# Kernel tuning notes

Measured on AMD Instinct MI355X. Metric: run time of the kernel, lower is better.

The kernel has to match this reference:

```python
import jax, jax.numpy as jnp
import numpy as np

TEMPERATURE = 8.0  # sqrt(head_dim=64)


def sparsemax(z):
    """Sparsemax along the last axis (Martins & Astudillo 2016)."""
    S = z.shape[-1]
    z_sorted = -jnp.sort(-z, axis=-1)            # descending sort
    cs = jnp.cumsum(z_sorted, axis=-1)
    ks = jnp.arange(1, S + 1, dtype=z.dtype)
    support = 1.0 + ks * z_sorted > cs           # entries in the support set
    k_sup = jnp.sum(support, axis=-1, keepdims=True)  # support size >= 1
    tau = (jnp.take_along_axis(cs, k_sup - 1, axis=-1) - 1.0) / k_sup.astype(z.dtype)
    return jnp.maximum(z - tau, 0.0)


def setup_inputs() -> dict:
    key = jax.random.key(0)
    kq, kk, kv, km = jax.random.split(key, 4)
    B, Lq, Lk, D = 64, 1024, 1024, 64
    q = jax.random.normal(kq, (B, Lq, D), dtype=jnp.float32)
    k = jax.random.normal(kk, (B, Lk, D), dtype=jnp.float32)
    v = jax.random.normal(kv, (B, Lk, D), dtype=jnp.float32)
    mask = jax.random.randint(km, (B, Lq, Lk), 0, 2).astype(bool)  # True = masked out
    return {"q": q, "k": k, "v": v, "mask": mask}


def reference(q, k, v, mask):
    # scores: [B, Lq, Lk]
    attn = jnp.einsum('bqd,bkd->bqk', q / TEMPERATURE, k)
    # mask out disallowed keys with -inf
    attn = jnp.where(mask, -jnp.inf, attn)
    # rows where ALL keys are masked: set scores to 0 (avoids NaN in sparsemax)
    inf_mask = jnp.all(mask, axis=2, keepdims=True)  # [B, Lq, 1]
    attn = jnp.where(inf_mask, 0.0, attn)
    attn = sparsemax(attn)
    # zero out fully-masked rows again (dropout has p=0.0 -> identity in eval)
    attn = jnp.where(inf_mask, 0.0, attn)
    out = jnp.einsum('bqk,bkd->bqd', attn, v)
    return (out, attn)
```

## Files before the change

kernel.cpp:

```cpp
#include <hip/hip_runtime.h>
#include <float.h>


#define BATCH    64
#define SEQQ     1024
#define SEQK     1024
#define DHEAD    64

typedef short short8 __attribute__((ext_vector_type(8)));
typedef float f32x4  __attribute__((ext_vector_type(4)));

__device__ __forceinline__ unsigned short bf16_rne(float f) {
    unsigned u = __float_as_uint(f);
    u += 0x7fffu + ((u >> 16) & 1u);
    return (unsigned short)(u >> 16);
}

__device__ __forceinline__ void cvt_hilo8(const float* fv, float scale,
                                          short8* hi, short8* lo) {
    #pragma unroll
    for (int j = 0; j < 8; ++j) {
        float f = fv[j] * scale;
        unsigned short hb = bf16_rne(f);
        float hf = __uint_as_float((unsigned)hb << 16);
        (*hi)[j] = (short)hb;
        (*lo)[j] = (short)bf16_rne(f - hf);
    }
}

__global__ void detect_mask_fmt(const unsigned char* __restrict__ m,
                                int* __restrict__ flag) {
    __shared__ int s_found;
    if (threadIdx.x == 0) s_found = 0;
    __syncthreads();
    int found = 0;
    for (int o = threadIdx.x; o < 65536; o += 256) {
        if ((o & 3) != 0 && m[o] != 0) found = 1;
    }
    if (found) atomicOr(&s_found, 1);
    __syncthreads();
    if (threadIdx.x == 0) *flag = s_found;
}

__global__ __launch_bounds__(256) void score_kernel(
        const float* __restrict__ q, const float* __restrict__ k,
        unsigned short* __restrict__ sbuf, int pitch) {
    const int lane = threadIdx.x & 63;
    const int wave = threadIdx.x >> 6;
    const int quad = lane >> 4;
    const int l15  = lane & 15;
    const int kt = blockIdx.x, qt = blockIdx.y, b = blockIdx.z;

    __shared__ unsigned short klds[2 * 128 * 64];

    const float* kbase = k + ((size_t)b * SEQK + kt * 128) * DHEAD;
    #pragma unroll
    for (int it = 0; it < 4; ++it) {
        int e   = threadIdx.x + 256 * it;
        int key = e >> 3, db = e & 7;
        const float4* src = (const float4*)(kbase + key * DHEAD + db * 8);
        float4 f0 = src[0], f1 = src[1];
        float fv[8] = {f0.x, f0.y, f0.z, f0.w, f1.x, f1.y, f1.z, f1.w};
        short8 hi, lo;
        cvt_hilo8(fv, 1.0f, &hi, &lo);
        int off = key * 64 + ((db ^ (key & 7)) * 8);
        *(short8*)(klds + off)        = hi;
        *(short8*)(klds + 8192 + off) = lo;
    }
    __syncthreads();

    const float* qrow =
        q + ((size_t)b * SEQQ + qt * 64 + wave * 16 + l15) * DHEAD;
    short8 a_hi[2], a_lo[2];
    #pragma unroll
    for (int kc = 0; kc < 2; ++kc) {
        const float4* src = (const float4*)(qrow + kc * 32 + quad * 8);
        float4 f0 = src[0], f1 = src[1];
        float fv[8] = {f0.x, f0.y, f0.z, f0.w, f1.x, f1.y, f1.z, f1.w};
        cvt_hilo8(fv, 0.125f, &a_hi[kc], &a_lo[kc]);
    }

    unsigned short* srow =
        sbuf + ((size_t)b * SEQQ + qt * 64 + wave * 16) * (size_t)pitch
             + kt * 128;
    #pragma unroll
    for (int g = 0; g < 8; ++g) {
        int key = g * 16 + l15;
        short8 b_hi[2], b_lo[2];
        #pragma unroll
        for (int kc = 0; kc < 2; ++kc) {
            int db  = kc * 4 + quad;
            int off = key * 64 + ((db ^ (key & 7)) * 8);
            b_hi[kc] = *(const short8*)(klds + off);
            b_lo[kc] = *(const short8*)(klds + 8192 + off);
        }
        f32x4 acc = {0.f, 0.f, 0.f, 0.f};
        #pragma unroll
        for (int kc = 0; kc < 2; ++kc) {
            acc = __builtin_amdgcn_mfma_f32_16x16x32_bf16(a_hi[kc], b_hi[kc], acc, 0, 0, 0);
            acc = __builtin_amdgcn_mfma_f32_16x16x32_bf16(a_lo[kc], b_hi[kc], acc, 0, 0, 0);
            acc = __builtin_amdgcn_mfma_f32_16x16x32_bf16(a_hi[kc], b_lo[kc], acc, 0, 0, 0);
        }
        #pragma unroll
        for (int r = 0; r < 4; ++r)
            srow[(size_t)(quad * 4 + r) * (size_t)pitch + g * 16 + l15] =
                bf16_rne(acc[r]);
    }
}

__global__ __launch_bounds__(256) void sparsemax_pv(
        const float* __restrict__ v, const void* __restrict__ mask,
        const int* __restrict__ fmt_flag,
        float* __restrict__ out, float* __restrict__ attn,
        const unsigned short* __restrict__ sbuf, int pitch) {
    const int lane = threadIdx.x & 63;
    const int wave = threadIdx.x >> 6;
    const int row  = blockIdx.x * 4 + wave;
    const int b    = row >> 10;
    float* arow = attn + (size_t)row * SEQK;
    const int mask_is_byte = fmt_flag ? *fmt_flag : 1;

    const ushort4* s4 =
        (const ushort4*)(sbuf + (size_t)row * (size_t)pitch);
    float s[16];
    #pragma unroll
    for (int t = 0; t < 4; ++t) {
        ushort4 u = s4[lane + 64 * t];
        s[4*t+0] = __uint_as_float((unsigned)u.x << 16);
        s[4*t+1] = __uint_as_float((unsigned)u.y << 16);
        s[4*t+2] = __uint_as_float((unsigned)u.z << 16);
        s[4*t+3] = __uint_as_float((unsigned)u.w << 16);
    }
    if (mask_is_byte) {
        const unsigned* m32 =
            (const unsigned*)((const unsigned char*)mask + (size_t)row * SEQK);
        #pragma unroll
        for (int t = 0; t < 4; ++t) {
            unsigned m = m32[lane + 64 * t];
            if (m & 0x000000ffu) s[4*t+0] = -FLT_MAX;
            if (m & 0x0000ff00u) s[4*t+1] = -FLT_MAX;
            if (m & 0x00ff0000u) s[4*t+2] = -FLT_MAX;
            if (m & 0xff000000u) s[4*t+3] = -FLT_MAX;
        }
    } else {
        const int4* m4 = (const int4*)((const int*)mask + (size_t)row * SEQK);
        #pragma unroll
        for (int t = 0; t < 4; ++t) {
            int4 m = m4[lane + 64 * t];
            if (m.x) s[4*t+0] = -FLT_MAX;
            if (m.y) s[4*t+1] = -FLT_MAX;
            if (m.z) s[4*t+2] = -FLT_MAX;
            if (m.w) s[4*t+3] = -FLT_MAX;
        }
    }

    float mx = -FLT_MAX;
    #pragma unroll
    for (int i = 0; i < 16; ++i) mx = fmaxf(mx, s[i]);
    #pragma unroll
    for (int off = 32; off >= 1; off >>= 1)
        mx = fmaxf(mx, __shfl_xor(mx, off, 64));

    if (mx <= -FLT_MAX) {
        float4 z = {0.f, 0.f, 0.f, 0.f};
        #pragma unroll
        for (int t = 0; t < 4; ++t) ((float4*)arow)[lane + 64 * t] = z;
        out[(size_t)row * DHEAD + lane] = 0.f;
        return;
    }

    float thr = mx - 1.0f, tau = 0.f;
    int cnt_prev = -1;
    for (int it = 0; it < 32; ++it) {
        float lsum = 0.f; int lcnt = 0;
        #pragma unroll
        for (int i = 0; i < 16; ++i)
            if (s[i] > thr) { lsum += s[i]; lcnt++; }
        #pragma unroll
        for (int off = 32; off >= 1; off >>= 1) {
            lsum += __shfl_xor(lsum, off, 64);
            lcnt += __shfl_xor(lcnt, off, 64);
        }
        tau = (lsum - 1.0f) / (float)lcnt;
        if (lcnt == cnt_prev) break;
        cnt_prev = lcnt;
        thr = tau;
    }

    float p[16];
    #pragma unroll
    for (int i = 0; i < 16; ++i) {
        float pv = s[i] - tau;
        p[i] = pv > 0.f ? pv : 0.f;
    }
    #pragma unroll
    for (int t = 0; t < 4; ++t) {
        float4 f = {p[4*t+0], p[4*t+1], p[4*t+2], p[4*t+3]};
        ((float4*)arow)[lane + 64 * t] = f;
    }

    const float* vbase = v + (size_t)b * SEQK * DHEAD;
    float oacc = 0.f;
    #pragma unroll
    for (int t = 0; t < 4; ++t) {
        #pragma unroll
        for (int c = 0; c < 4; ++c) {
            int i = 4 * t + c;
            unsigned long long mball = __ballot(p[i] > 0.f);
            while (mball) {
                int src = __ffsll(mball) - 1;
                mball &= mball - 1;
                float pj = __shfl(p[i], src);
                int key = 4 * (src + 64 * t) + c;
                oacc = fmaf(pj, vbase[(size_t)key * DHEAD + lane], oacc);
            }
        }
    }
    out[(size_t)row * DHEAD + lane] = oacc;
}

extern "C" void kernel_launch(void* const* d_in, const int* in_sizes, int n_in,
                              void* d_out, int out_size, void* d_ws, size_t ws_size,
                              hipStream_t stream) {
    const float* q = (const float*)d_in[0];
    const float* k = (const float*)d_in[1];
    const float* v = (const float*)d_in[2];
    const void*  m = d_in[3];

    float* out  = (float*)d_out;
    float* attn = out + (size_t)BATCH * SEQQ * DHEAD;

    int* flag = nullptr;
    if (ws_size >= sizeof(int)) {
        flag = (int*)d_ws;
        detect_mask_fmt<<<1, 256, 0, stream>>>((const unsigned char*)m, flag);
    }

    const size_t s_elems = (size_t)BATCH * SEQQ * SEQK;
    unsigned short* sbuf;
    int pitch;
    if (ws_size >= 16 + s_elems * sizeof(unsigned short)) {
        sbuf  = (unsigned short*)d_ws + 8;
        pitch = SEQK;
    } else {
        sbuf  = (unsigned short*)attn;
        pitch = 2 * SEQK;
    }

    dim3 gridA(SEQK / 128, SEQQ / 64, BATCH);
    score_kernel<<<gridA, 256, 0, stream>>>(q, k, sbuf, pitch);

    sparsemax_pv<<<(BATCH * SEQQ) / 4, 256, 0, stream>>>(
        v, m, flag, out, attn, sbuf, pitch);
}
```

Measured before the change: 695.8 us.

## Loop key tiles inside score blocks, batch PV gathers, and stream attention stores

```diff
diff --git a/kernel.cpp b/kernel.cpp
--- a/kernel.cpp
+++ b/kernel.cpp
@@ -49,25 +49,10 @@
     const int wave = threadIdx.x >> 6;
     const int quad = lane >> 4;
     const int l15  = lane & 15;
-    const int kt = blockIdx.x, qt = blockIdx.y, b = blockIdx.z;
+    const int qt = blockIdx.x >> 6;
+    const int b  = blockIdx.x & 63;
 
     __shared__ unsigned short klds[2 * 128 * 64];
-
-    const float* kbase = k + ((size_t)b * SEQK + kt * 128) * DHEAD;
-    #pragma unroll
-    for (int it = 0; it < 4; ++it) {
-        int e   = threadIdx.x + 256 * it;
-        int key = e >> 3, db = e & 7;
-        const float4* src = (const float4*)(kbase + key * DHEAD + db * 8);
-        float4 f0 = src[0], f1 = src[1];
-        float fv[8] = {f0.x, f0.y, f0.z, f0.w, f1.x, f1.y, f1.z, f1.w};
-        short8 hi, lo;
-        cvt_hilo8(fv, 1.0f, &hi, &lo);
-        int off = key * 64 + ((db ^ (key & 7)) * 8);
-        *(short8*)(klds + off)        = hi;
-        *(short8*)(klds + 8192 + off) = lo;
-    }
-    __syncthreads();
 
     const float* qrow =
         q + ((size_t)b * SEQQ + qt * 64 + wave * 16 + l15) * DHEAD;
@@ -80,31 +65,52 @@
         cvt_hilo8(fv, 0.125f, &a_hi[kc], &a_lo[kc]);
     }
 
-    unsigned short* srow =
-        sbuf + ((size_t)b * SEQQ + qt * 64 + wave * 16) * (size_t)pitch
-             + kt * 128;
-    #pragma unroll
-    for (int g = 0; g < 8; ++g) {
-        int key = g * 16 + l15;
-        short8 b_hi[2], b_lo[2];
-        #pragma unroll
-        for (int kc = 0; kc < 2; ++kc) {
-            int db  = kc * 4 + quad;
+    const float* kb = k + (size_t)b * SEQK * DHEAD;
+    unsigned short* srow0 =
+        sbuf + ((size_t)b * SEQQ + qt * 64 + wave * 16) * (size_t)pitch;
+
+    for (int kt = 0; kt < 8; ++kt) {
+        __syncthreads();
+        const float* kbase = kb + (size_t)kt * 128 * DHEAD;
+        #pragma unroll
+        for (int it = 0; it < 4; ++it) {
+            int e   = threadIdx.x + 256 * it;
+            int key = e >> 3, db = e & 7;
+            const float4* src = (const float4*)(kbase + key * DHEAD + db * 8);
+            float4 f0 = src[0], f1 = src[1];
+            float fv[8] = {f0.x, f0.y, f0.z, f0.w, f1.x, f1.y, f1.z, f1.w};
+            short8 hi, lo;
+            cvt_hilo8(fv, 1.0f, &hi, &lo);
             int off = key * 64 + ((db ^ (key & 7)) * 8);
-            b_hi[kc] = *(const short8*)(klds + off);
-            b_lo[kc] = *(const short8*)(klds + 8192 + off);
-        }
-        f32x4 acc = {0.f, 0.f, 0.f, 0.f};
-        #pragma unroll
-        for (int kc = 0; kc < 2; ++kc) {
-            acc = __builtin_amdgcn_mfma_f32_16x16x32_bf16(a_hi[kc], b_hi[kc], acc, 0, 0, 0);
-            acc = __builtin_amdgcn_mfma_f32_16x16x32_bf16(a_lo[kc], b_hi[kc], acc, 0, 0, 0);
-            acc = __builtin_amdgcn_mfma_f32_16x16x32_bf16(a_hi[kc], b_lo[kc], acc, 0, 0, 0);
-        }
-        #pragma unroll
-        for (int r = 0; r < 4; ++r)
-            srow[(size_t)(quad * 4 + r) * (size_t)pitch + g * 16 + l15] =
-                bf16_rne(acc[r]);
+            *(short8*)(klds + off)        = hi;
+            *(short8*)(klds + 8192 + off) = lo;
+        }
+        __syncthreads();
+
+        unsigned short* srow = srow0 + kt * 128;
+        #pragma unroll
+        for (int g = 0; g < 8; ++g) {
+            int key = g * 16 + l15;
+            short8 b_hi[2], b_lo[2];
+            #pragma unroll
+            for (int kc = 0; kc < 2; ++kc) {
+                int db  = kc * 4 + quad;
+                int off = key * 64 + ((db ^ (key & 7)) * 8);
+                b_hi[kc] = *(const short8*)(klds + off);
+                b_lo[kc] = *(const short8*)(klds + 8192 + off);
+            }
+            f32x4 acc = {0.f, 0.f, 0.f, 0.f};
+            #pragma unroll
+            for (int kc = 0; kc < 2; ++kc) {
+                acc = __builtin_amdgcn_mfma_f32_16x16x32_bf16(a_hi[kc], b_hi[kc], acc, 0, 0, 0);
+                acc = __builtin_amdgcn_mfma_f32_16x16x32_bf16(a_lo[kc], b_hi[kc], acc, 0, 0, 0);
+                acc = __builtin_amdgcn_mfma_f32_16x16x32_bf16(a_hi[kc], b_lo[kc], acc, 0, 0, 0);
+            }
+            #pragma unroll
+            for (int r = 0; r < 4; ++r)
+                srow[(size_t)(quad * 4 + r) * (size_t)pitch + g * 16 + l15] =
+                    bf16_rne(acc[r]);
+        }
     }
 }
 
@@ -120,6 +126,8 @@
     float* arow = attn + (size_t)row * SEQK;
     const int mask_is_byte = fmt_flag ? *fmt_flag : 1;
 
+    __shared__ float pbuf[4][SEQK];
+
     const ushort4* s4 =
         (const ushort4*)(sbuf + (size_t)row * (size_t)pitch);
     float s[16];
@@ -162,9 +170,10 @@
         mx = fmaxf(mx, __shfl_xor(mx, off, 64));
 
     if (mx <= -FLT_MAX) {
-        float4 z = {0.f, 0.f, 0.f, 0.f};
-        #pragma unroll
-        for (int t = 0; t < 4; ++t) ((float4*)arow)[lane + 64 * t] = z;
+        f32x4 z = {0.f, 0.f, 0.f, 0.f};
+        #pragma unroll
+        for (int t = 0; t < 4; ++t)
+            __builtin_nontemporal_store(z, (f32x4*)arow + lane + 64 * t);
         out[(size_t)row * DHEAD + lane] = 0.f;
         return;
     }
@@ -195,8 +204,9 @@
     }
     #pragma unroll
     for (int t = 0; t < 4; ++t) {
-        float4 f = {p[4*t+0], p[4*t+1], p[4*t+2], p[4*t+3]};
-        ((float4*)arow)[lane + 64 * t] = f;
+        f32x4 f = {p[4*t+0], p[4*t+1], p[4*t+2], p[4*t+3]};
+        __builtin_nontemporal_store(f, (f32x4*)arow + lane + 64 * t);
+        *(f32x4*)&pbuf[wave][4 * (lane + 64 * t)] = f;
     }
 
     const float* vbase = v + (size_t)b * SEQK * DHEAD;
@@ -206,13 +216,37 @@
         #pragma unroll
         for (int c = 0; c < 4; ++c) {
             int i = 4 * t + c;
-            unsigned long long mball = __ballot(p[i] > 0.f);
-            while (mball) {
-                int src = __ffsll(mball) - 1;
-                mball &= mball - 1;
-                float pj = __shfl(p[i], src);
-                int key = 4 * (src + 64 * t) + c;
-                oacc = fmaf(pj, vbase[(size_t)key * DHEAD + lane], oacc);
+            unsigned long long mb = __ballot(p[i] > 0.f);
+            while (mb) {
+                int k0, k1 = -1, k2 = -1, k3 = -1;
+                k0 = __ffsll(mb) - 1; mb &= mb - 1;
+                if (mb) { k1 = __ffsll(mb) - 1; mb &= mb - 1; }
+                if (mb) { k2 = __ffsll(mb) - 1; mb &= mb - 1; }
+                if (mb) { k3 = __ffsll(mb) - 1; mb &= mb - 1; }
+                int key0 = 4 * k0 + 256 * t + c;
+                float pj0 = pbuf[wave][key0];
+                float v0  = vbase[(size_t)key0 * DHEAD + lane];
+                float pj1 = 0.f, pj2 = 0.f, pj3 = 0.f;
+                float v1 = 0.f, v2 = 0.f, v3 = 0.f;
+                if (k1 >= 0) {
+                    int key1 = 4 * k1 + 256 * t + c;
+                    pj1 = pbuf[wave][key1];
+                    v1  = vbase[(size_t)key1 * DHEAD + lane];
+                }
+                if (k2 >= 0) {
+                    int key2 = 4 * k2 + 256 * t + c;
+                    pj2 = pbuf[wave][key2];
+                    v2  = vbase[(size_t)key2 * DHEAD + lane];
+                }
+                if (k3 >= 0) {
+                    int key3 = 4 * k3 + 256 * t + c;
+                    pj3 = pbuf[wave][key3];
+                    v3  = vbase[(size_t)key3 * DHEAD + lane];
+                }
+                oacc = fmaf(pj0, v0, oacc);
+                if (k1 >= 0) oacc = fmaf(pj1, v1, oacc);
+                if (k2 >= 0) oacc = fmaf(pj2, v2, oacc);
+                if (k3 >= 0) oacc = fmaf(pj3, v3, oacc);
             }
         }
     }
@@ -247,8 +281,7 @@
         pitch = 2 * SEQK;
     }
 
-    dim3 gridA(SEQK / 128, SEQQ / 64, BATCH);
-    score_kernel<<<gridA, 256, 0, stream>>>(q, k, sbuf, pitch);
+    score_kernel<<<(SEQQ / 64) * BATCH, 256, 0, stream>>>(q, k, sbuf, pitch);
 
     sparsemax_pv<<<(BATCH * SEQQ) / 4, 256, 0, stream>>>(
         v, m, flag, out, attn, sbuf, pitch);
```

After: 682.3 us. About the same (-1.9%).
